# Performance work log

Measured on AMD Instinct MI355X. Metric: run time of the kernel, lower is better.

## Reference

```python
import jax, jax.numpy as jnp
import numpy as np


def make_coord(h, w):
    # grid-center coords in (-1, 1), order (y, x), flattened [h*w, 2]
    ry, rx = 1.0 / h, 1.0 / w
    ys = -1.0 + ry + 2.0 * ry * jnp.arange(h, dtype=jnp.float32)
    xs = -1.0 + rx + 2.0 * rx * jnp.arange(w, dtype=jnp.float32)
    gy, gx = jnp.meshgrid(ys, xs, indexing='ij')
    return jnp.stack([gy, gx], axis=-1).reshape(-1, 2)


def setup_inputs() -> dict:
    key = jax.random.key(0)
    ks = jax.random.split(key, 11)
    B, C, H, W = 4, 4, 256, 256
    d = 256
    inp = {
        'feat': jax.random.normal(ks[0], (B, C, H, W), dtype=jnp.float32),
        'W1': jax.random.normal(ks[1], (d, 4), dtype=jnp.float32) * 0.05,
        'b1': jax.random.normal(ks[2], (d,), dtype=jnp.float32) * 0.05,
        'W2': jax.random.normal(ks[3], (d, d), dtype=jnp.float32) * 0.05,
        'b2': jax.random.normal(ks[4], (d,), dtype=jnp.float32) * 0.05,
        'W3': jax.random.normal(ks[5], (d, d), dtype=jnp.float32) * 0.05,
        'b3': jax.random.normal(ks[6], (d,), dtype=jnp.float32) * 0.05,
        'W4': jax.random.normal(ks[7], (d, d), dtype=jnp.float32) * 0.05,
        'b4': jax.random.normal(ks[8], (d,), dtype=jnp.float32) * 0.05,
        'W5': jax.random.normal(ks[9], (12, d), dtype=jnp.float32) * 0.05,
        'b5': jax.random.normal(ks[10], (12,), dtype=jnp.float32) * 0.05,
    }
    return inp


def reference(feat, W1, b1, W2, b2, W3, b3, W4, b4, W5, b5):
    B, C, H, W = feat.shape
    q = H * W
    coord = make_coord(H, W)                                  # [q, 2] (y, x)
    scale = jnp.stack([jnp.full((q,), 1.0 / H, jnp.float32),
                       jnp.full((q,), 1.0 / W, jnp.float32)], axis=-1)

    # nearest grid_sample (align_corners=False): unnorm = (c+1)*n/2 - 0.5
    iy = jnp.clip(jnp.round((coord[:, 0] + 1.0) * H / 2.0 - 0.5), 0, H - 1).astype(jnp.int32)
    ix = jnp.clip(jnp.round((coord[:, 1] + 1.0) * W / 2.0 - 0.5), 0, W - 1).astype(jnp.int32)
    lin = iy * W + ix                                         # [q]

    value = jnp.take(feat.reshape(B, C, H * W), lin, axis=2)  # [B, C, q]
    value = value.transpose(0, 2, 1)                          # [B, q, C]
    coord_k = coord[lin]                                      # [q, 2] gathered feat centers

    hw = jnp.array([H, W], dtype=jnp.float32)
    rel = (coord - coord_k) * hw                              # [q, 2]
    scale_ = scale * hw                                       # [q, 2]
    inp = jnp.concatenate([rel, scale_], axis=-1)             # [q, 4]
    inp = jnp.broadcast_to(inp[None], (B, q, 4)).reshape(B * q, 4)

    x = inp
    for Wi, bi in ((W1, b1), (W2, b2), (W3, b3), (W4, b4)):
        x = jax.nn.gelu(x @ Wi.T + bi, approximate=False)
    weight = (x @ W5.T + b5).reshape(B * q, C, 3)             # per-query (C,3) weights

    pred = jnp.einsum('nc,ncd->nd', value.reshape(B * q, C), weight)
    return pred.reshape(B, q, 3)
```

## Files before the change

kernel.cpp:

```cpp
#include <hip/hip_runtime.h>

#define POISON 0xAAAAAAAAu
#define NMLP 16u

__device__ __forceinline__ float gelu_exact(float x) {
    return 0.5f * x * (1.0f + erff(x * 0.7071067811865475f));
}

__device__ __forceinline__ float dot4(float4 a, float4 b) {
    return a.x * b.x + a.y * b.y + a.z * b.z + a.w * b.w;
}

__device__ __forceinline__ void mlp_barrier(unsigned* slot) {
    __syncthreads();
    if (threadIdx.x == 0) {
        atomicCAS(slot, POISON, 0u);
        __threadfence();
        atomicAdd(slot, 1u);
        while (__hip_atomic_fetch_add(slot, 0u, __ATOMIC_ACQUIRE,
                                      __HIP_MEMORY_SCOPE_AGENT) < NMLP)
            __builtin_amdgcn_s_sleep(16);
    }
    __syncthreads();
}

__global__ __launch_bounds__(256) void mlp16_kernel(
    const float* __restrict__ W1, const float* __restrict__ b1,
    const float* __restrict__ W2, const float* __restrict__ b2,
    const float* __restrict__ W3, const float* __restrict__ b3,
    const float* __restrict__ W4, const float* __restrict__ b4,
    const float* __restrict__ W5, const float* __restrict__ b5,
    float* __restrict__ ws)
{
    float*    w12  = ws;
    unsigned* barA = (unsigned*)(ws + 32);
    unsigned* barB = (unsigned*)(ws + 64);
    float*    xb2  = ws + 128;
    float*    xb3  = ws + 384;

    __shared__ __align__(16) float xs[256];
    __shared__ float x4loc[16];

    const int t = threadIdx.x;
    const int m = blockIdx.x;
    const int q = t >> 4;
    const int c = t & 15;
    const int n = m * 16 + q;

    {
        float4 w1r = *reinterpret_cast<const float4*>(W1 + t * 4);
        xs[t] = gelu_exact(w1r.z + w1r.w + b1[t]);
    }
    __syncthreads();

    {
        float acc = 0.f;
        #pragma unroll
        for (int i = 0; i < 4; ++i) {
            float4 wv = *reinterpret_cast<const float4*>(W2 + (size_t)n * 256 + i * 64 + c * 4);
            float4 xv = *reinterpret_cast<const float4*>(xs + i * 64 + c * 4);
            acc += dot4(wv, xv);
        }
        #pragma unroll
        for (int off = 1; off <= 8; off <<= 1) acc += __shfl_xor(acc, off);
        if (c == 0)
            __hip_atomic_exchange(&xb2[n], gelu_exact(acc + b2[n]),
                                  __ATOMIC_RELEASE, __HIP_MEMORY_SCOPE_AGENT);
    }
    mlp_barrier(barA);

    xs[t] = xb2[t];
    __syncthreads();
    {
        float acc = 0.f;
        #pragma unroll
        for (int i = 0; i < 4; ++i) {
            float4 wv = *reinterpret_cast<const float4*>(W3 + (size_t)n * 256 + i * 64 + c * 4);
            float4 xv = *reinterpret_cast<const float4*>(xs + i * 64 + c * 4);
            acc += dot4(wv, xv);
        }
        #pragma unroll
        for (int off = 1; off <= 8; off <<= 1) acc += __shfl_xor(acc, off);
        if (c == 0)
            __hip_atomic_exchange(&xb3[n], gelu_exact(acc + b3[n]),
                                  __ATOMIC_RELEASE, __HIP_MEMORY_SCOPE_AGENT);
    }
    mlp_barrier(barB);

    xs[t] = xb3[t];
    __syncthreads();
    {
        float acc = 0.f;
        #pragma unroll
        for (int i = 0; i < 4; ++i) {
            float4 wv = *reinterpret_cast<const float4*>(W4 + (size_t)n * 256 + i * 64 + c * 4);
            float4 xv = *reinterpret_cast<const float4*>(xs + i * 64 + c * 4);
            acc += dot4(wv, xv);
        }
        #pragma unroll
        for (int off = 1; off <= 8; off <<= 1) acc += __shfl_xor(acc, off);
        if (c == 0) x4loc[q] = gelu_exact(acc + b4[n]);
    }
    __syncthreads();

    if (t < 12) {
        float acc = 0.f;
        #pragma unroll
        for (int qq = 0; qq < 16; ++qq)
            acc += x4loc[qq] * W5[(size_t)t * 256 + m * 16 + qq];
        if (m == 0) acc += b5[t];
        atomicCAS((unsigned*)&w12[t], POISON, 0u);
        atomicAdd(&w12[t], acc);
    }
}

__global__ __launch_bounds__(256) void apply_kernel(
    const float* __restrict__ feat, const float* __restrict__ w12,
    float* __restrict__ out)
{
    __shared__ float wl[12];
    const int t = threadIdx.x;
    if (t < 12) wl[t] = w12[t];
    __syncthreads();

    float wr[12];
    #pragma unroll
    for (int i = 0; i < 12; ++i) wr[i] = wl[i];

    const int idx = blockIdx.x * 256 + t;
    const int b   = idx >> 14;
    const int pos = (idx & 16383) << 2;

    const float* fb = feat + (size_t)b * 4 * 65536 + pos;
    const float4 f0 = *reinterpret_cast<const float4*>(fb);
    const float4 f1 = *reinterpret_cast<const float4*>(fb + 65536);
    const float4 f2 = *reinterpret_cast<const float4*>(fb + 131072);
    const float4 f3 = *reinterpret_cast<const float4*>(fb + 196608);

    float r[12];
    #pragma unroll
    for (int dd = 0; dd < 3; ++dd) {
        r[0 + dd] = f0.x * wr[dd] + f1.x * wr[3 + dd] + f2.x * wr[6 + dd] + f3.x * wr[9 + dd];
        r[3 + dd] = f0.y * wr[dd] + f1.y * wr[3 + dd] + f2.y * wr[6 + dd] + f3.y * wr[9 + dd];
        r[6 + dd] = f0.z * wr[dd] + f1.z * wr[3 + dd] + f2.z * wr[6 + dd] + f3.z * wr[9 + dd];
        r[9 + dd] = f0.w * wr[dd] + f1.w * wr[3 + dd] + f2.w * wr[6 + dd] + f3.w * wr[9 + dd];
    }

    float* op = out + (size_t)(b * 65536 + pos) * 3;
    reinterpret_cast<float4*>(op)[0] = make_float4(r[0], r[1], r[2],  r[3]);
    reinterpret_cast<float4*>(op)[1] = make_float4(r[4], r[5], r[6],  r[7]);
    reinterpret_cast<float4*>(op)[2] = make_float4(r[8], r[9], r[10], r[11]);
}

extern "C" void kernel_launch(void* const* d_in, const int* in_sizes, int n_in,
                              void* d_out, int out_size, void* d_ws, size_t ws_size,
                              hipStream_t stream) {
    const float* feat = (const float*)d_in[0];
    const float* W1   = (const float*)d_in[1];
    const float* b1   = (const float*)d_in[2];
    const float* W2   = (const float*)d_in[3];
    const float* b2   = (const float*)d_in[4];
    const float* W3   = (const float*)d_in[5];
    const float* b3   = (const float*)d_in[6];
    const float* W4   = (const float*)d_in[7];
    const float* b4   = (const float*)d_in[8];
    const float* W5   = (const float*)d_in[9];
    const float* b5   = (const float*)d_in[10];

    float* out = (float*)d_out;
    float* ws  = (float*)d_ws;

    mlp16_kernel<<<NMLP, 256, 0, stream>>>(W1, b1, W2, b2, W3, b3, W4, b4,
                                           W5, b5, ws);
    apply_kernel<<<256, 256, 0, stream>>>(feat, ws, out);
}
```

Baseline: 83.82 us.

## Fuse MLP and apply kernels into one launch with a device-side completion flag

Merges the 16-block MLP kernel and the 256-block apply kernel into a single launch. The apply blocks load their feature data early, then spin on a global done counter until the MLP blocks have finished the 12 weights. The MLP blocks also prefetch W3 and W4 rows into registers before each grid barrier, and the barrier sleep interval is shortened. This removes a kernel launch gap and overlaps feature loads with the MLP. It relies on every block being co-resident, since apply blocks spin while waiting on the MLP blocks.

```diff
diff --git a/kernel.cpp b/kernel.cpp
--- a/kernel.cpp
+++ b/kernel.cpp
@@ -1,7 +1,7 @@
 #include <hip/hip_runtime.h>
 
 #define POISON 0xAAAAAAAAu
-#define NMLP 16u
+#define NMLP 16
 
 __device__ __forceinline__ float gelu_exact(float x) {
     return 0.5f * x * (1.0f + erff(x * 0.7071067811865475f));
@@ -19,115 +19,121 @@
         atomicAdd(slot, 1u);
         while (__hip_atomic_fetch_add(slot, 0u, __ATOMIC_ACQUIRE,
                                       __HIP_MEMORY_SCOPE_AGENT) < NMLP)
-            __builtin_amdgcn_s_sleep(16);
+            __builtin_amdgcn_s_sleep(8);
     }
     __syncthreads();
 }
 
-__global__ __launch_bounds__(256) void mlp16_kernel(
+__global__ __launch_bounds__(256) void fused4_kernel(
     const float* __restrict__ W1, const float* __restrict__ b1,
     const float* __restrict__ W2, const float* __restrict__ b2,
     const float* __restrict__ W3, const float* __restrict__ b3,
     const float* __restrict__ W4, const float* __restrict__ b4,
     const float* __restrict__ W5, const float* __restrict__ b5,
+    const float* __restrict__ feat, float* __restrict__ out,
     float* __restrict__ ws)
 {
     float*    w12  = ws;
-    unsigned* barA = (unsigned*)(ws + 32);
-    unsigned* barB = (unsigned*)(ws + 64);
+    unsigned* done = (unsigned*)(ws + 32);
+    unsigned* barA = (unsigned*)(ws + 64);
+    unsigned* barB = (unsigned*)(ws + 96);
     float*    xb2  = ws + 128;
     float*    xb3  = ws + 384;
 
     __shared__ __align__(16) float xs[256];
     __shared__ float x4loc[16];
+    __shared__ float wl[12];
 
     const int t = threadIdx.x;
     const int m = blockIdx.x;
-    const int q = t >> 4;
-    const int c = t & 15;
-    const int n = m * 16 + q;
 
-    {
-        float4 w1r = *reinterpret_cast<const float4*>(W1 + t * 4);
-        xs[t] = gelu_exact(w1r.z + w1r.w + b1[t]);
+    if (m < NMLP) {
+        const int q = t >> 4;
+        const int c = t & 15;
+        const int n = m * 16 + q;
+
+        {
+            float4 w1r = *reinterpret_cast<const float4*>(W1 + t * 4);
+            xs[t] = gelu_exact(w1r.z + w1r.w + b1[t]);
+        }
+        __syncthreads();
+
+        float4 w3r[4];
+        {
+            float acc = 0.f;
+            #pragma unroll
+            for (int i = 0; i < 4; ++i) {
+                float4 wv = *reinterpret_cast<const float4*>(W2 + (size_t)n * 256 + i * 64 + c * 4);
+                float4 xv = *reinterpret_cast<const float4*>(xs + i * 64 + c * 4);
+                acc += dot4(wv, xv);
+            }
+            #pragma unroll
+            for (int i = 0; i < 4; ++i)
+                w3r[i] = *reinterpret_cast<const float4*>(W3 + (size_t)n * 256 + i * 64 + c * 4);
+            #pragma unroll
+            for (int off = 1; off <= 8; off <<= 1) acc += __shfl_xor(acc, off);
+            if (c == 0)
+                __hip_atomic_exchange(&xb2[n], gelu_exact(acc + b2[n]),
+                                      __ATOMIC_RELEASE, __HIP_MEMORY_SCOPE_AGENT);
+        }
+        mlp_barrier(barA);
+
+        xs[t] = xb2[t];
+        __syncthreads();
+        float4 w4r[4];
+        {
+            float acc = 0.f;
+            #pragma unroll
+            for (int i = 0; i < 4; ++i) {
+                float4 xv = *reinterpret_cast<const float4*>(xs + i * 64 + c * 4);
+                acc += dot4(w3r[i], xv);
+            }
+            #pragma unroll
+            for (int i = 0; i < 4; ++i)
+                w4r[i] = *reinterpret_cast<const float4*>(W4 + (size_t)n * 256 + i * 64 + c * 4);
+            #pragma unroll
+            for (int off = 1; off <= 8; off <<= 1) acc += __shfl_xor(acc, off);
+            if (c == 0)
+                __hip_atomic_exchange(&xb3[n], gelu_exact(acc + b3[n]),
+                                      __ATOMIC_RELEASE, __HIP_MEMORY_SCOPE_AGENT);
+        }
+        mlp_barrier(barB);
+
+        xs[t] = xb3[t];
+        __syncthreads();
+        {
+            float acc = 0.f;
+            #pragma unroll
+            for (int i = 0; i < 4; ++i) {
+                float4 xv = *reinterpret_cast<const float4*>(xs + i * 64 + c * 4);
+                acc += dot4(w4r[i], xv);
+            }
+            #pragma unroll
+            for (int off = 1; off <= 8; off <<= 1) acc += __shfl_xor(acc, off);
+            if (c == 0) x4loc[q] = gelu_exact(acc + b4[n]);
+        }
+        __syncthreads();
+
+        if (t < 12) {
+            float acc = 0.f;
+            #pragma unroll
+            for (int qq = 0; qq < 16; ++qq)
+                acc += x4loc[qq] * W5[(size_t)t * 256 + m * 16 + qq];
+            if (m == 0) acc += b5[t];
+            atomicCAS((unsigned*)&w12[t], POISON, 0u);
+            atomicAdd(&w12[t], acc);
+        }
+        __syncthreads();
+        if (t == 0) {
+            atomicCAS(done, POISON, 0u);
+            __hip_atomic_fetch_add(done, 1u, __ATOMIC_RELEASE,
+                                   __HIP_MEMORY_SCOPE_AGENT);
+        }
+        return;
     }
-    __syncthreads();
 
-    {
-        float acc = 0.f;
-        #pragma unroll
-        for (int i = 0; i < 4; ++i) {
-            float4 wv = *reinterpret_cast<const float4*>(W2 + (size_t)n * 256 + i * 64 + c * 4);
-            float4 xv = *reinterpret_cast<const float4*>(xs + i * 64 + c * 4);
-            acc += dot4(wv, xv);
-        }
-        #pragma unroll
-        for (int off = 1; off <= 8; off <<= 1) acc += __shfl_xor(acc, off);
-        if (c == 0)
-            __hip_atomic_exchange(&xb2[n], gelu_exact(acc + b2[n]),
-                                  __ATOMIC_RELEASE, __HIP_MEMORY_SCOPE_AGENT);
-    }
-    mlp_barrier(barA);
-
-    xs[t] = xb2[t];
-    __syncthreads();
-    {
-        float acc = 0.f;
-        #pragma unroll
-        for (int i = 0; i < 4; ++i) {
-            float4 wv = *reinterpret_cast<const float4*>(W3 + (size_t)n * 256 + i * 64 + c * 4);
-            float4 xv = *reinterpret_cast<const float4*>(xs + i * 64 + c * 4);
-            acc += dot4(wv, xv);
-        }
-        #pragma unroll
-        for (int off = 1; off <= 8; off <<= 1) acc += __shfl_xor(acc, off);
-        if (c == 0)
-            __hip_atomic_exchange(&xb3[n], gelu_exact(acc + b3[n]),
-                                  __ATOMIC_RELEASE, __HIP_MEMORY_SCOPE_AGENT);
-    }
-    mlp_barrier(barB);
-
-    xs[t] = xb3[t];
-    __syncthreads();
-    {
-        float acc = 0.f;
-        #pragma unroll
-        for (int i = 0; i < 4; ++i) {
-            float4 wv = *reinterpret_cast<const float4*>(W4 + (size_t)n * 256 + i * 64 + c * 4);
-            float4 xv = *reinterpret_cast<const float4*>(xs + i * 64 + c * 4);
-            acc += dot4(wv, xv);
-        }
-        #pragma unroll
-        for (int off = 1; off <= 8; off <<= 1) acc += __shfl_xor(acc, off);
-        if (c == 0) x4loc[q] = gelu_exact(acc + b4[n]);
-    }
-    __syncthreads();
-
-    if (t < 12) {
-        float acc = 0.f;
-        #pragma unroll
-        for (int qq = 0; qq < 16; ++qq)
-            acc += x4loc[qq] * W5[(size_t)t * 256 + m * 16 + qq];
-        if (m == 0) acc += b5[t];
-        atomicCAS((unsigned*)&w12[t], POISON, 0u);
-        atomicAdd(&w12[t], acc);
-    }
-}
-
-__global__ __launch_bounds__(256) void apply_kernel(
-    const float* __restrict__ feat, const float* __restrict__ w12,
-    float* __restrict__ out)
-{
-    __shared__ float wl[12];
-    const int t = threadIdx.x;
-    if (t < 12) wl[t] = w12[t];
-    __syncthreads();
-
-    float wr[12];
-    #pragma unroll
-    for (int i = 0; i < 12; ++i) wr[i] = wl[i];
-
-    const int idx = blockIdx.x * 256 + t;
+    const int a   = m - NMLP;
+    const int idx = a * 256 + t;
     const int b   = idx >> 14;
     const int pos = (idx & 16383) << 2;
 
@@ -136,6 +142,21 @@
     const float4 f1 = *reinterpret_cast<const float4*>(fb + 65536);
     const float4 f2 = *reinterpret_cast<const float4*>(fb + 131072);
     const float4 f3 = *reinterpret_cast<const float4*>(fb + 196608);
+
+    if (t == 0) {
+        while (__hip_atomic_fetch_add(done, 0u, __ATOMIC_RELAXED,
+                                      __HIP_MEMORY_SCOPE_AGENT) != (unsigned)NMLP)
+            __builtin_amdgcn_s_sleep(16);
+    }
+    __syncthreads();
+    if (t < 12)
+        wl[t] = __hip_atomic_fetch_add(&w12[t], 0.0f, __ATOMIC_RELAXED,
+                                       __HIP_MEMORY_SCOPE_AGENT);
+    __syncthreads();
+
+    float wr[12];
+    #pragma unroll
+    for (int i = 0; i < 12; ++i) wr[i] = wl[i];
 
     float r[12];
     #pragma unroll
@@ -170,7 +191,6 @@
     float* out = (float*)d_out;
     float* ws  = (float*)d_ws;
 
-    mlp16_kernel<<<NMLP, 256, 0, stream>>>(W1, b1, W2, b2, W3, b3, W4, b4,
-                                           W5, b5, ws);
-    apply_kernel<<<256, 256, 0, stream>>>(feat, ws, out);
+    fused4_kernel<<<NMLP + 256, 256, 0, stream>>>(W1, b1, W2, b2, W3, b3,
+                                                  W4, b4, W5, b5, feat, out, ws);
 }
```

Result: slower. 88.29 us (+5.3%).

## Replace grid spin barriers with split-K kernel chain and fuse final layer into apply

Applied to the files above, without the earlier changes.

Removes the atomic spin-wait grid barriers in the MLP kernel by splitting the layers into three kernels that pass split-K partial sums through workspace. Each apply block redundantly reduces the last partials and computes the 12 output weights locally, eliminating the atomicAdd accumulation. The feat loads are issued before the MLP tail so they overlap. This adds one kernel launch and redundant per-block work in exchange.

```diff
diff --git a/kernel.cpp b/kernel.cpp
--- a/kernel.cpp
+++ b/kernel.cpp
@@ -1,7 +1,4 @@
 #include <hip/hip_runtime.h>
-
-#define POISON 0xAAAAAAAAu
-#define NMLP 16u
 
 __device__ __forceinline__ float gelu_exact(float x) {
     return 0.5f * x * (1.0f + erff(x * 0.7071067811865475f));
@@ -11,131 +8,139 @@
     return a.x * b.x + a.y * b.y + a.z * b.z + a.w * b.w;
 }
 
-__device__ __forceinline__ void mlp_barrier(unsigned* slot) {
-    __syncthreads();
-    if (threadIdx.x == 0) {
-        atomicCAS(slot, POISON, 0u);
-        __threadfence();
-        atomicAdd(slot, 1u);
-        while (__hip_atomic_fetch_add(slot, 0u, __ATOMIC_ACQUIRE,
-                                      __HIP_MEMORY_SCOPE_AGENT) < NMLP)
-            __builtin_amdgcn_s_sleep(16);
-    }
-    __syncthreads();
-}
 
-__global__ __launch_bounds__(256) void mlp16_kernel(
+__global__ __launch_bounds__(256) void k1_kernel(
     const float* __restrict__ W1, const float* __restrict__ b1,
     const float* __restrict__ W2, const float* __restrict__ b2,
-    const float* __restrict__ W3, const float* __restrict__ b3,
-    const float* __restrict__ W4, const float* __restrict__ b4,
-    const float* __restrict__ W5, const float* __restrict__ b5,
-    float* __restrict__ ws)
+    const float* __restrict__ W3, float* __restrict__ ws)
 {
-    float*    w12  = ws;
-    unsigned* barA = (unsigned*)(ws + 32);
-    unsigned* barB = (unsigned*)(ws + 64);
-    float*    xb2  = ws + 128;
-    float*    xb3  = ws + 384;
-
-    __shared__ __align__(16) float xs[256];
-    __shared__ float x4loc[16];
+    float* z3p = ws;
+    __shared__ __align__(16) float x1l[256];
+    __shared__ __align__(16) float x2l[16];
 
     const int t = threadIdx.x;
     const int m = blockIdx.x;
     const int q = t >> 4;
     const int c = t & 15;
-    const int n = m * 16 + q;
 
     {
         float4 w1r = *reinterpret_cast<const float4*>(W1 + t * 4);
-        xs[t] = gelu_exact(w1r.z + w1r.w + b1[t]);
+        x1l[t] = gelu_exact(w1r.z + w1r.w + b1[t]);
     }
     __syncthreads();
 
     {
+        const int n = m * 16 + q;
         float acc = 0.f;
         #pragma unroll
         for (int i = 0; i < 4; ++i) {
-            float4 wv = *reinterpret_cast<const float4*>(W2 + (size_t)n * 256 + i * 64 + c * 4);
-            float4 xv = *reinterpret_cast<const float4*>(xs + i * 64 + c * 4);
+            float4 wv = *reinterpret_cast<const float4*>(W2 + (size_t)n * 256 + c * 16 + i * 4);
+            float4 xv = *reinterpret_cast<const float4*>(x1l + c * 16 + i * 4);
             acc += dot4(wv, xv);
         }
         #pragma unroll
         for (int off = 1; off <= 8; off <<= 1) acc += __shfl_xor(acc, off);
-        if (c == 0)
-            __hip_atomic_exchange(&xb2[n], gelu_exact(acc + b2[n]),
-                                  __ATOMIC_RELEASE, __HIP_MEMORY_SCOPE_AGENT);
-    }
-    mlp_barrier(barA);
-
-    xs[t] = xb2[t];
-    __syncthreads();
-    {
-        float acc = 0.f;
-        #pragma unroll
-        for (int i = 0; i < 4; ++i) {
-            float4 wv = *reinterpret_cast<const float4*>(W3 + (size_t)n * 256 + i * 64 + c * 4);
-            float4 xv = *reinterpret_cast<const float4*>(xs + i * 64 + c * 4);
-            acc += dot4(wv, xv);
-        }
-        #pragma unroll
-        for (int off = 1; off <= 8; off <<= 1) acc += __shfl_xor(acc, off);
-        if (c == 0)
-            __hip_atomic_exchange(&xb3[n], gelu_exact(acc + b3[n]),
-                                  __ATOMIC_RELEASE, __HIP_MEMORY_SCOPE_AGENT);
-    }
-    mlp_barrier(barB);
-
-    xs[t] = xb3[t];
-    __syncthreads();
-    {
-        float acc = 0.f;
-        #pragma unroll
-        for (int i = 0; i < 4; ++i) {
-            float4 wv = *reinterpret_cast<const float4*>(W4 + (size_t)n * 256 + i * 64 + c * 4);
-            float4 xv = *reinterpret_cast<const float4*>(xs + i * 64 + c * 4);
-            acc += dot4(wv, xv);
-        }
-        #pragma unroll
-        for (int off = 1; off <= 8; off <<= 1) acc += __shfl_xor(acc, off);
-        if (c == 0) x4loc[q] = gelu_exact(acc + b4[n]);
+        if (c == 0) x2l[q] = gelu_exact(acc + b2[n]);
     }
     __syncthreads();
 
-    if (t < 12) {
-        float acc = 0.f;
+    {
+        float a3 = 0.f;
         #pragma unroll
-        for (int qq = 0; qq < 16; ++qq)
-            acc += x4loc[qq] * W5[(size_t)t * 256 + m * 16 + qq];
-        if (m == 0) acc += b5[t];
-        atomicCAS((unsigned*)&w12[t], POISON, 0u);
-        atomicAdd(&w12[t], acc);
+        for (int i = 0; i < 4; ++i) {
+            float4 wv = *reinterpret_cast<const float4*>(W3 + (size_t)t * 256 + m * 16 + i * 4);
+            float4 xv = *reinterpret_cast<const float4*>(x2l + i * 4);
+            a3 += dot4(wv, xv);
+        }
+        z3p[m * 256 + t] = a3;
     }
 }
 
-__global__ __launch_bounds__(256) void apply_kernel(
-    const float* __restrict__ feat, const float* __restrict__ w12,
-    float* __restrict__ out)
+__global__ __launch_bounds__(256) void k2_kernel(
+    const float* __restrict__ b3, const float* __restrict__ W4,
+    float* __restrict__ ws)
 {
+    const float* z3p = ws;
+    float*       z4p = ws + 4096;
+    __shared__ float zred[256];
+    __shared__ __align__(16) float x3l[16];
+
+    const int t = threadIdx.x;
+    const int m = blockIdx.x;
+    const int j = t >> 4;
+    const int i = t & 15;
+
+    zred[t] = z3p[j * 256 + m * 16 + i];
+    __syncthreads();
+    if (t < 16) {
+        float s = 0.f;
+        #pragma unroll
+        for (int jj = 0; jj < 16; ++jj) s += zred[jj * 16 + t];
+        x3l[t] = gelu_exact(s + b3[m * 16 + t]);
+    }
+    __syncthreads();
+
+    {
+        float a4 = 0.f;
+        #pragma unroll
+        for (int ii = 0; ii < 4; ++ii) {
+            float4 wv = *reinterpret_cast<const float4*>(W4 + (size_t)t * 256 + m * 16 + ii * 4);
+            float4 xv = *reinterpret_cast<const float4*>(x3l + ii * 4);
+            a4 += dot4(wv, xv);
+        }
+        z4p[m * 256 + t] = a4;
+    }
+}
+
+__global__ __launch_bounds__(256) void k3_kernel(
+    const float* __restrict__ b4, const float* __restrict__ W5,
+    const float* __restrict__ b5, const float* __restrict__ feat,
+    float* __restrict__ out, const float* __restrict__ ws)
+{
+    const float* z4p = ws + 4096;
+    __shared__ __align__(16) float x4l[256];
     __shared__ float wl[12];
+
     const int t = threadIdx.x;
-    if (t < 12) wl[t] = w12[t];
+
+    const int idx = blockIdx.x * 256 + t;
+    const int b   = idx >> 14;
+    const int pos = (idx & 16383) << 2;
+    const float* fb = feat + (size_t)b * 4 * 65536 + pos;
+    const float4 f0 = *reinterpret_cast<const float4*>(fb);
+    const float4 f1 = *reinterpret_cast<const float4*>(fb + 65536);
+    const float4 f2 = *reinterpret_cast<const float4*>(fb + 131072);
+    const float4 f3 = *reinterpret_cast<const float4*>(fb + 196608);
+
+    {
+        float s = b4[t];
+        #pragma unroll
+        for (int j = 0; j < 16; ++j) s += z4p[j * 256 + t];
+        x4l[t] = gelu_exact(s);
+    }
+    __syncthreads();
+
+    {
+        const int q = t >> 4;
+        const int c = t & 15;
+        if (q < 12) {
+            float acc = 0.f;
+            #pragma unroll
+            for (int i = 0; i < 4; ++i) {
+                float4 wv = *reinterpret_cast<const float4*>(W5 + (size_t)q * 256 + c * 16 + i * 4);
+                float4 xv = *reinterpret_cast<const float4*>(x4l + c * 16 + i * 4);
+                acc += dot4(wv, xv);
+            }
+            #pragma unroll
+            for (int off = 1; off <= 8; off <<= 1) acc += __shfl_xor(acc, off);
+            if (c == 0) wl[q] = acc + b5[q];
+        }
+    }
     __syncthreads();
 
     float wr[12];
     #pragma unroll
     for (int i = 0; i < 12; ++i) wr[i] = wl[i];
-
-    const int idx = blockIdx.x * 256 + t;
-    const int b   = idx >> 14;
-    const int pos = (idx & 16383) << 2;
-
-    const float* fb = feat + (size_t)b * 4 * 65536 + pos;
-    const float4 f0 = *reinterpret_cast<const float4*>(fb);
-    const float4 f1 = *reinterpret_cast<const float4*>(fb + 65536);
-    const float4 f2 = *reinterpret_cast<const float4*>(fb + 131072);
-    const float4 f3 = *reinterpret_cast<const float4*>(fb + 196608);
 
     float r[12];
     #pragma unroll
@@ -170,7 +175,7 @@
     float* out = (float*)d_out;
     float* ws  = (float*)d_ws;
 
-    mlp16_kernel<<<NMLP, 256, 0, stream>>>(W1, b1, W2, b2, W3, b3, W4, b4,
-                                           W5, b5, ws);
-    apply_kernel<<<256, 256, 0, stream>>>(feat, ws, out);
+    k1_kernel<<<16, 256, 0, stream>>>(W1, b1, W2, b2, W3, ws);
+    k2_kernel<<<16, 256, 0, stream>>>(b3, W4, ws);
+    k3_kernel<<<256, 256, 0, stream>>>(b4, W5, b5, feat, out, ws);
 }
```

Result: faster. 82.16 us (-2.0%).
